# Kernel optimization log

Hardware: AMD Instinct MI355X
Metric: run time of the kernel (lower is better)

The kernel has to match this reference:

```python
import jax, jax.numpy as jnp
import numpy as np

N_NODES = 50000
N_EDGES = 600000
N_GRAPHS = 256
IN_C = 128
HID = 128
OUT_C = 2


def setup_inputs() -> dict:
    key = jax.random.key(0)
    ks = jax.random.split(key, 16)
    d = {}
    d["x"] = jax.random.normal(ks[0], (N_NODES, IN_C), jnp.float32)
    d["edge_index"] = jax.random.randint(ks[1], (2, N_EDGES), 0, N_NODES, dtype=jnp.int32)
    d["root_node_idx"] = jax.random.randint(ks[2], (N_GRAPHS,), 0, N_NODES, dtype=jnp.int32)
    d["batch"] = jnp.sort(jax.random.randint(ks[3], (N_NODES,), 0, N_GRAPHS, dtype=jnp.int32))
    dims = [(IN_C, HID), (HID, HID), (HID, HID), (HID, HID)]
    for i, (ci, co) in enumerate(dims, start=1):
        s = 1.0 / np.sqrt(ci)
        d[f"w{i}_l"] = jax.random.uniform(ks[3 + i], (co, ci), jnp.float32, -s, s)
        d[f"b{i}_l"] = jnp.zeros((co,), jnp.float32)
        d[f"w{i}_r"] = jax.random.uniform(ks[7 + i], (co, ci), jnp.float32, -s, s)
    s = 1.0 / np.sqrt(2 * HID)
    d["w_cls"] = jax.random.uniform(ks[12], (OUT_C, 2 * HID), jnp.float32, -s, s)
    d["b_cls"] = jnp.zeros((OUT_C,), jnp.float32)
    return d


def _sage_conv(x, src, tgt, deg_inv, w_l, b_l, w_r):
    # mean aggregation of source features at target nodes (PyG SAGEConv, aggr='mean')
    agg = jax.ops.segment_sum(x[src], tgt, num_segments=N_NODES) * deg_inv  # [N, C]
    # out = lin_l(agg) + lin_r(x); lin_r has no bias in PyG SAGEConv
    return agg @ w_l.T + b_l + x @ w_r.T


def reference(x, edge_index, root_node_idx, batch,
              w1_l, b1_l, w1_r, w2_l, b2_l, w2_r,
              w3_l, b3_l, w3_r, w4_l, b4_l, w4_r,
              w_cls, b_cls):
    src, tgt = edge_index[0], edge_index[1]
    ones_e = jnp.ones((src.shape[0],), x.dtype)
    deg = jax.ops.segment_sum(ones_e, tgt, num_segments=N_NODES)
    deg_inv = (1.0 / jnp.maximum(deg, 1.0))[:, None]  # [N, 1]

    h = jax.nn.relu(_sage_conv(x, src, tgt, deg_inv, w1_l, b1_l, w1_r))
    h = jax.nn.relu(_sage_conv(h, src, tgt, deg_inv, w2_l, b2_l, w2_r))
    h = jax.nn.relu(_sage_conv(h, src, tgt, deg_inv, w3_l, b3_l, w3_r))
    h = jax.nn.relu(_sage_conv(h, src, tgt, deg_inv, w4_l, b4_l, w4_r))

    root_emb = h[root_node_idx]  # [G, HID]
    g_sum = jax.ops.segment_sum(h, batch, num_segments=N_GRAPHS)
    g_cnt = jax.ops.segment_sum(jnp.ones((h.shape[0],), h.dtype), batch, num_segments=N_GRAPHS)
    graph_emb = g_sum / jnp.maximum(g_cnt, 1.0)[:, None]  # [G, HID]

    combined = jnp.concatenate([root_emb, graph_emb], axis=1)  # [G, 2*HID]
    return combined @ w_cls.T + b_cls  # [G, OUT_C]
```

## Files before the change

kernel.cpp:

```cpp
#include <hip/hip_runtime.h>
#include <hip/hip_bf16.h>

#define N_NODES 50000
#define N_EDGES 600000
#define N_GRAPHS 256
#define C 128
#define NB 196

typedef unsigned short ushort;
typedef unsigned int uint;
typedef __attribute__((ext_vector_type(8))) short bfrag8;
typedef __attribute__((ext_vector_type(4))) float facc4;

__device__ __forceinline__ ushort f2bf(float v) {
    uint u = __float_as_uint(v);
    u += 0x7FFFu + ((u >> 16) & 1u);
    return (ushort)(u >> 16);
}
__device__ __forceinline__ float bf2f(ushort u) {
    return __uint_as_float(((uint)u) << 16);
}
__device__ __forceinline__ void fsplit(float v, ushort& h, ushort& l) {
    h = f2bf(v);
    l = f2bf(v - bf2f(h));
}

__global__ void k_deg(const int* __restrict__ tgt, int* __restrict__ deg) {
    int e = blockIdx.x * blockDim.x + threadIdx.x;
    if (e < N_EDGES) atomicAdd(&deg[tgt[e]], 1);
}

__global__ __launch_bounds__(256) void k_bsum(const int* __restrict__ deg,
                                              int* __restrict__ bsum,
                                              float* __restrict__ dinv) {
    __shared__ int ws[4];
    int idx = blockIdx.x * 256 + threadIdx.x;
    int v = (idx < N_NODES) ? deg[idx] : 0;
    if (idx < N_NODES) dinv[idx] = 1.0f / fmaxf((float)v, 1.0f);
    int s = v;
#pragma unroll
    for (int off = 1; off < 64; off <<= 1) s += __shfl_xor(s, off);
    if ((threadIdx.x & 63) == 0) ws[threadIdx.x >> 6] = s;
    __syncthreads();
    if (threadIdx.x == 0) bsum[blockIdx.x] = ws[0] + ws[1] + ws[2] + ws[3];
}

__global__ __launch_bounds__(256) void k_bscan(const int* __restrict__ bsum,
                                               int* __restrict__ boff,
                                               int* __restrict__ rowptr) {
    __shared__ int ws[4];
    int t = threadIdx.x, lane = t & 63, w = t >> 6;
    int v = (t < NB) ? bsum[t] : 0;
    int incl = v;
#pragma unroll
    for (int off = 1; off < 64; off <<= 1) {
        int u = __shfl_up(incl, off);
        if (lane >= off) incl += u;
    }
    if (lane == 63) ws[w] = incl;
    __syncthreads();
    int wo = 0;
    if (w > 0) wo += ws[0];
    if (w > 1) wo += ws[1];
    if (w > 2) wo += ws[2];
    if (t < NB) boff[t] = wo + incl - v;
    if (t == 0) rowptr[N_NODES] = N_EDGES;
}

__global__ __launch_bounds__(256) void k_rowptr(const int* __restrict__ deg,
                                                const int* __restrict__ boff,
                                                int* __restrict__ rowptr) {
    __shared__ int ws[4];
    int b = blockIdx.x, t = threadIdx.x;
    int idx = b * 256 + t;
    int lane = t & 63, w = t >> 6;
    int v = (idx < N_NODES) ? deg[idx] : 0;
    int incl = v;
#pragma unroll
    for (int off = 1; off < 64; off <<= 1) {
        int u = __shfl_up(incl, off);
        if (lane >= off) incl += u;
    }
    if (lane == 63) ws[w] = incl;
    __syncthreads();
    int wo = 0;
    if (w > 0) wo += ws[0];
    if (w > 1) wo += ws[1];
    if (w > 2) wo += ws[2];
    if (idx < N_NODES) rowptr[idx] = boff[b] + wo + incl - v;
}

__global__ void k_fill(const int* __restrict__ src, const int* __restrict__ tgt,
                       const int* __restrict__ rowptr, int* __restrict__ fill,
                       int* __restrict__ csr_src) {
    int e = blockIdx.x * blockDim.x + threadIdx.x;
    if (e >= N_EDGES) return;
    int d = tgt[e];
    int pos = atomicAdd(&fill[d], 1);
    csr_src[rowptr[d] + pos] = src[e];
}

__global__ __launch_bounds__(256) void k_xsplit(const float* __restrict__ x,
                                                ushort* __restrict__ Ahi,
                                                ushort* __restrict__ Alo) {
    int gid = blockIdx.x * 256 + threadIdx.x;
    if (gid >= N_NODES * 32) return;
    int n = gid >> 5, c4 = (gid & 31) << 2;
    float4 v = *(const float4*)(x + (size_t)n * C + c4);
    ushort4 h, l;
    fsplit(v.x, h.x, l.x); fsplit(v.y, h.y, l.y);
    fsplit(v.z, h.z, l.z); fsplit(v.w, h.w, l.w);
    *(ushort4*)(Ahi + (size_t)n * 256 + 128 + c4) = h;
    *(ushort4*)(Alo + (size_t)n * 256 + 128 + c4) = l;
}

struct WPtrs { const float* wl[4]; const float* wr[4]; };
__global__ __launch_bounds__(256) void k_wsplit(WPtrs wp, ushort* __restrict__ BTh,
                                                ushort* __restrict__ BTl) {
    int gid = blockIdx.x * 256 + threadIdx.x;
    if (gid >= 4 * 128 * 256) return;
    int l = gid >> 15;
    int rem = gid & 32767;
    int n = rem >> 8, k = rem & 255;
    float v = (k < 128) ? wp.wl[l][n * 128 + k] : wp.wr[l][n * 128 + (k - 128)];
    ushort h, lo;
    fsplit(v, h, lo);
    BTh[gid] = h;
    BTl[gid] = lo;
}

__global__ __launch_bounds__(256) void k_gather(const ushort* __restrict__ Ahi_r,
                                                const ushort* __restrict__ Alo_r,
                                                ushort* __restrict__ Ahi_w,
                                                ushort* __restrict__ Alo_w,
                                                const int* __restrict__ csr_src,
                                                const int* __restrict__ rowptr,
                                                const float* __restrict__ dinv) {
    int node = blockIdx.x * 8 + (threadIdx.x >> 5);
    if (node >= N_NODES) return;
    int lane = threadIdx.x & 31;
    int c4 = lane << 2;
    int s = rowptr[node], e = rowptr[node + 1];
    float a0 = 0.f, a1 = 0.f, a2 = 0.f, a3 = 0.f;
    int j = s;
    for (; j + 3 < e; j += 4) {
        int s0 = csr_src[j], s1 = csr_src[j + 1];
        int s2 = csr_src[j + 2], s3 = csr_src[j + 3];
        ushort4 h0 = *(const ushort4*)(Ahi_r + (size_t)s0 * 256 + 128 + c4);
        ushort4 l0 = *(const ushort4*)(Alo_r + (size_t)s0 * 256 + 128 + c4);
        ushort4 h1 = *(const ushort4*)(Ahi_r + (size_t)s1 * 256 + 128 + c4);
        ushort4 l1 = *(const ushort4*)(Alo_r + (size_t)s1 * 256 + 128 + c4);
        ushort4 h2 = *(const ushort4*)(Ahi_r + (size_t)s2 * 256 + 128 + c4);
        ushort4 l2 = *(const ushort4*)(Alo_r + (size_t)s2 * 256 + 128 + c4);
        ushort4 h3 = *(const ushort4*)(Ahi_r + (size_t)s3 * 256 + 128 + c4);
        ushort4 l3 = *(const ushort4*)(Alo_r + (size_t)s3 * 256 + 128 + c4);
        a0 += (bf2f(h0.x) + bf2f(l0.x)) + (bf2f(h1.x) + bf2f(l1.x))
            + (bf2f(h2.x) + bf2f(l2.x)) + (bf2f(h3.x) + bf2f(l3.x));
        a1 += (bf2f(h0.y) + bf2f(l0.y)) + (bf2f(h1.y) + bf2f(l1.y))
            + (bf2f(h2.y) + bf2f(l2.y)) + (bf2f(h3.y) + bf2f(l3.y));
        a2 += (bf2f(h0.z) + bf2f(l0.z)) + (bf2f(h1.z) + bf2f(l1.z))
            + (bf2f(h2.z) + bf2f(l2.z)) + (bf2f(h3.z) + bf2f(l3.z));
        a3 += (bf2f(h0.w) + bf2f(l0.w)) + (bf2f(h1.w) + bf2f(l1.w))
            + (bf2f(h2.w) + bf2f(l2.w)) + (bf2f(h3.w) + bf2f(l3.w));
    }
    for (; j < e; j++) {
        int s0 = csr_src[j];
        ushort4 h0 = *(const ushort4*)(Ahi_r + (size_t)s0 * 256 + 128 + c4);
        ushort4 l0 = *(const ushort4*)(Alo_r + (size_t)s0 * 256 + 128 + c4);
        a0 += bf2f(h0.x) + bf2f(l0.x);
        a1 += bf2f(h0.y) + bf2f(l0.y);
        a2 += bf2f(h0.z) + bf2f(l0.z);
        a3 += bf2f(h0.w) + bf2f(l0.w);
    }
    float sc = dinv[node];
    a0 *= sc; a1 *= sc; a2 *= sc; a3 *= sc;
    ushort4 h, l;
    fsplit(a0, h.x, l.x); fsplit(a1, h.y, l.y);
    fsplit(a2, h.z, l.z); fsplit(a3, h.w, l.w);
    *(ushort4*)(Ahi_w + (size_t)node * 256 + c4) = h;
    *(ushort4*)(Alo_w + (size_t)node * 256 + c4) = l;
}

__global__ __launch_bounds__(256) void k_gemm(const ushort* __restrict__ Ahi,
                                              const ushort* __restrict__ Alo,
                                              const ushort* __restrict__ BTh,
                                              const ushort* __restrict__ BTl,
                                              const float* __restrict__ bl,
                                              ushort* __restrict__ Hhi,
                                              ushort* __restrict__ Hlo) {
    __shared__ short As[2][128][40];
    __shared__ short Bs[2][128][40];
    const int tid = threadIdx.x;
    const int wave = tid >> 6, lane = tid & 63;
    const int m0 = blockIdx.x * 128;
    const int wm = (wave & 1) * 64;
    const int wn = (wave >> 1) * 64;
    const int l15 = lane & 15, lk = (lane >> 4) * 8;

    const int sr = tid >> 1;
    const int sc = (tid & 1) * 16;
    int garow = m0 + sr; if (garow >= N_NODES) garow = N_NODES - 1;
    const ushort* pAh = Ahi + (size_t)garow * 256 + sc;
    const ushort* pAl = Alo + (size_t)garow * 256 + sc;
    const ushort* pBh = BTh + sr * 256 + sc;
    const ushort* pBl = BTl + sr * 256 + sc;

    bfrag8 rAh0, rAh1, rAl0, rAl1, rBh0, rBh1, rBl0, rBl1;
#define LOADSTEP(K0) do { \
        rAh0 = *(const bfrag8*)(pAh + (K0));     rAh1 = *(const bfrag8*)(pAh + (K0) + 8); \
        rAl0 = *(const bfrag8*)(pAl + (K0));     rAl1 = *(const bfrag8*)(pAl + (K0) + 8); \
        rBh0 = *(const bfrag8*)(pBh + (K0));     rBh1 = *(const bfrag8*)(pBh + (K0) + 8); \
        rBl0 = *(const bfrag8*)(pBl + (K0));     rBl1 = *(const bfrag8*)(pBl + (K0) + 8); \
    } while (0)

    LOADSTEP(0);
    facc4 acc[4][4] = {};
#pragma unroll
    for (int s = 0; s < 8; s++) {
        *(bfrag8*)&As[0][sr][sc]     = rAh0;  *(bfrag8*)&As[0][sr][sc + 8] = rAh1;
        *(bfrag8*)&As[1][sr][sc]     = rAl0;  *(bfrag8*)&As[1][sr][sc + 8] = rAl1;
        *(bfrag8*)&Bs[0][sr][sc]     = rBh0;  *(bfrag8*)&Bs[0][sr][sc + 8] = rBh1;
        *(bfrag8*)&Bs[1][sr][sc]     = rBl0;  *(bfrag8*)&Bs[1][sr][sc + 8] = rBl1;
        __syncthreads();
        if (s < 7) LOADSTEP((s + 1) * 32);
        bfrag8 a[2][4], b[2][4];
#pragma unroll
        for (int t = 0; t < 4; t++) {
            a[0][t] = *(const bfrag8*)&As[0][wm + t * 16 + l15][lk];
            a[1][t] = *(const bfrag8*)&As[1][wm + t * 16 + l15][lk];
            b[0][t] = *(const bfrag8*)&Bs[0][wn + t * 16 + l15][lk];
            b[1][t] = *(const bfrag8*)&Bs[1][wn + t * 16 + l15][lk];
        }
#pragma unroll
        for (int mt = 0; mt < 4; mt++)
#pragma unroll
            for (int nt = 0; nt < 4; nt++) {
                acc[mt][nt] = __builtin_amdgcn_mfma_f32_16x16x32_bf16(a[0][mt], b[0][nt], acc[mt][nt], 0, 0, 0);
                acc[mt][nt] = __builtin_amdgcn_mfma_f32_16x16x32_bf16(a[0][mt], b[1][nt], acc[mt][nt], 0, 0, 0);
                acc[mt][nt] = __builtin_amdgcn_mfma_f32_16x16x32_bf16(a[1][mt], b[0][nt], acc[mt][nt], 0, 0, 0);
            }
        __syncthreads();
    }
#undef LOADSTEP

    const int r4 = (lane >> 4) * 4;
#pragma unroll
    for (int mt = 0; mt < 4; mt++) {
#pragma unroll
        for (int nt = 0; nt < 4; nt++) {
            int col = wn + nt * 16 + l15;
            float bias = bl[col];
#pragma unroll
            for (int r = 0; r < 4; r++) {
                int grow = m0 + wm + mt * 16 + r4 + r;
                if (grow < N_NODES) {
                    float v = fmaxf(acc[mt][nt][r] + bias, 0.f);
                    ushort h, l;
                    fsplit(v, h, l);
                    Hhi[(size_t)grow * 256 + 128 + col] = h;
                    Hlo[(size_t)grow * 256 + 128 + col] = l;
                }
            }
        }
    }
}

__global__ void k_gstart(const int* __restrict__ batch, int* __restrict__ gstart) {
    int g = blockIdx.x * blockDim.x + threadIdx.x;
    if (g > N_GRAPHS) return;
    int lo = 0, hi = N_NODES;
    while (lo < hi) {
        int mid = (lo + hi) >> 1;
        if (batch[mid] < g) lo = mid + 1;
        else hi = mid;
    }
    gstart[g] = lo;
}

__global__ __launch_bounds__(512) void k_pool(const ushort* __restrict__ Ahi,
                                              const ushort* __restrict__ Alo,
                                              const int* __restrict__ gstart,
                                              float* __restrict__ gmean) {
    __shared__ float part[4][C];
    int g = blockIdx.x;
    int c = threadIdx.x & 127, p = threadIdx.x >> 7;
    int s = gstart[g], e = gstart[g + 1];
    float sum = 0.f;
    for (int n = s + p; n < e; n += 4) {
        size_t o = (size_t)n * 256 + 128 + c;
        sum += bf2f(Ahi[o]) + bf2f(Alo[o]);
    }
    part[p][c] = sum;
    __syncthreads();
    if (p == 0) {
        float tot = part[0][c] + part[1][c] + part[2][c] + part[3][c];
        float cnt = fmaxf((float)(e - s), 1.0f);
        gmean[g * C + c] = tot / cnt;
    }
}

__global__ __launch_bounds__(256) void k_final(const ushort* __restrict__ Ahi,
                                               const ushort* __restrict__ Alo,
                                               const float* __restrict__ gmean,
                                               const int* __restrict__ root,
                                               const float* __restrict__ wcls,
                                               const float* __restrict__ bcls,
                                               float* __restrict__ out) {
    __shared__ float red[8];
    int g = blockIdx.x, t = threadIdx.x;
    float v;
    if (t < 128) {
        size_t o = (size_t)root[g] * 256 + 128 + t;
        v = bf2f(Ahi[o]) + bf2f(Alo[o]);
    } else {
        v = gmean[g * C + (t - 128)];
    }
    float p0 = v * wcls[t];
    float p1 = v * wcls[256 + t];
#pragma unroll
    for (int off = 32; off; off >>= 1) {
        p0 += __shfl_down(p0, off);
        p1 += __shfl_down(p1, off);
    }
    int wid = t >> 6;
    if ((t & 63) == 0) { red[wid] = p0; red[4 + wid] = p1; }
    __syncthreads();
    if (t == 0) {
        out[g * 2 + 0] = red[0] + red[1] + red[2] + red[3] + bcls[0];
        out[g * 2 + 1] = red[4] + red[5] + red[6] + red[7] + bcls[1];
    }
}

extern "C" void kernel_launch(void* const* d_in, const int* in_sizes, int n_in,
                              void* d_out, int out_size, void* d_ws, size_t ws_size,
                              hipStream_t stream) {
    const float* x = (const float*)d_in[0];
    const int* ei = (const int*)d_in[1];
    const int* src = ei;
    const int* tgt = ei + N_EDGES;
    const int* root = (const int*)d_in[2];
    const int* batch = (const int*)d_in[3];
    WPtrs wp;
    wp.wl[0] = (const float*)d_in[4];  wp.wr[0] = (const float*)d_in[6];
    wp.wl[1] = (const float*)d_in[7];  wp.wr[1] = (const float*)d_in[9];
    wp.wl[2] = (const float*)d_in[10]; wp.wr[2] = (const float*)d_in[12];
    wp.wl[3] = (const float*)d_in[13]; wp.wr[3] = (const float*)d_in[15];
    const float* blv[4] = {(const float*)d_in[5], (const float*)d_in[8],
                           (const float*)d_in[11], (const float*)d_in[14]};
    const float* wcls = (const float*)d_in[16];
    const float* bcls = (const float*)d_in[17];
    float* out = (float*)d_out;

    ushort* Ahi = (ushort*)d_ws;
    ushort* Alo = Ahi + (size_t)N_NODES * 256;
    ushort* BTh = Alo + (size_t)N_NODES * 256;
    ushort* BTl = BTh + 4 * 128 * 256;
    int* deg = (int*)(BTl + 4 * 128 * 256);
    float* dinv = (float*)(deg + N_NODES);
    int* rowptr = (int*)(dinv + N_NODES);
    int* fill = rowptr + N_NODES + 1;
    int* csr_src = fill + N_NODES;
    int* bsum = csr_src + N_EDGES;
    int* boff = bsum + 256;
    int* gstart = boff + 256;
    float* gmean = (float*)(gstart + 260);

    hipMemsetAsync(deg, 0, N_NODES * sizeof(int), stream);
    hipMemsetAsync(fill, 0, N_NODES * sizeof(int), stream);
    k_deg<<<(N_EDGES + 255) / 256, 256, 0, stream>>>(tgt, deg);
    k_bsum<<<NB, 256, 0, stream>>>(deg, bsum, dinv);
    k_bscan<<<1, 256, 0, stream>>>(bsum, boff, rowptr);
    k_rowptr<<<NB, 256, 0, stream>>>(deg, boff, rowptr);
    k_fill<<<(N_EDGES + 255) / 256, 256, 0, stream>>>(src, tgt, rowptr, fill, csr_src);
    k_gstart<<<1, 512, 0, stream>>>(batch, gstart);
    k_xsplit<<<(N_NODES * 32 + 255) / 256, 256, 0, stream>>>(x, Ahi, Alo);
    k_wsplit<<<(4 * 128 * 256 + 255) / 256, 256, 0, stream>>>(wp, BTh, BTl);

    for (int l = 0; l < 4; l++) {
        k_gather<<<(N_NODES + 7) / 8, 256, 0, stream>>>(Ahi, Alo, Ahi, Alo,
                                                        csr_src, rowptr, dinv);
        k_gemm<<<(N_NODES + 127) / 128, 256, 0, stream>>>(
            Ahi, Alo, BTh + l * 32768, BTl + l * 32768, blv[l], Ahi, Alo);
    }
    k_pool<<<N_GRAPHS, 512, 0, stream>>>(Ahi, Alo, gstart, gmean);
    k_final<<<N_GRAPHS, 256, 0, stream>>>(Ahi, Alo, gmean, root, wcls, bcls, out);
}
```

Measured before the change: 486.4 us.

## Widen gather loads to 16 bytes and restage GEMM A tiles in MFMA fragment order

```diff
diff --git a/kernel.cpp b/kernel.cpp
--- a/kernel.cpp
+++ b/kernel.cpp
@@ -136,49 +136,50 @@
                                                 const int* __restrict__ csr_src,
                                                 const int* __restrict__ rowptr,
                                                 const float* __restrict__ dinv) {
-    int node = blockIdx.x * 8 + (threadIdx.x >> 5);
+    int node = blockIdx.x * 16 + (threadIdx.x >> 4);
     if (node >= N_NODES) return;
-    int lane = threadIdx.x & 31;
-    int c4 = lane << 2;
+    int c8 = (threadIdx.x & 15) << 3;
     int s = rowptr[node], e = rowptr[node + 1];
-    float a0 = 0.f, a1 = 0.f, a2 = 0.f, a3 = 0.f;
+    float a[8] = {0.f, 0.f, 0.f, 0.f, 0.f, 0.f, 0.f, 0.f};
     int j = s;
     for (; j + 3 < e; j += 4) {
         int s0 = csr_src[j], s1 = csr_src[j + 1];
         int s2 = csr_src[j + 2], s3 = csr_src[j + 3];
-        ushort4 h0 = *(const ushort4*)(Ahi_r + (size_t)s0 * 256 + 128 + c4);
-        ushort4 l0 = *(const ushort4*)(Alo_r + (size_t)s0 * 256 + 128 + c4);
-        ushort4 h1 = *(const ushort4*)(Ahi_r + (size_t)s1 * 256 + 128 + c4);
-        ushort4 l1 = *(const ushort4*)(Alo_r + (size_t)s1 * 256 + 128 + c4);
-        ushort4 h2 = *(const ushort4*)(Ahi_r + (size_t)s2 * 256 + 128 + c4);
-        ushort4 l2 = *(const ushort4*)(Alo_r + (size_t)s2 * 256 + 128 + c4);
-        ushort4 h3 = *(const ushort4*)(Ahi_r + (size_t)s3 * 256 + 128 + c4);
-        ushort4 l3 = *(const ushort4*)(Alo_r + (size_t)s3 * 256 + 128 + c4);
-        a0 += (bf2f(h0.x) + bf2f(l0.x)) + (bf2f(h1.x) + bf2f(l1.x))
-            + (bf2f(h2.x) + bf2f(l2.x)) + (bf2f(h3.x) + bf2f(l3.x));
-        a1 += (bf2f(h0.y) + bf2f(l0.y)) + (bf2f(h1.y) + bf2f(l1.y))
-            + (bf2f(h2.y) + bf2f(l2.y)) + (bf2f(h3.y) + bf2f(l3.y));
-        a2 += (bf2f(h0.z) + bf2f(l0.z)) + (bf2f(h1.z) + bf2f(l1.z))
-            + (bf2f(h2.z) + bf2f(l2.z)) + (bf2f(h3.z) + bf2f(l3.z));
-        a3 += (bf2f(h0.w) + bf2f(l0.w)) + (bf2f(h1.w) + bf2f(l1.w))
-            + (bf2f(h2.w) + bf2f(l2.w)) + (bf2f(h3.w) + bf2f(l3.w));
+        bfrag8 h0 = *(const bfrag8*)(Ahi_r + (size_t)s0 * 256 + 128 + c8);
+        bfrag8 l0 = *(const bfrag8*)(Alo_r + (size_t)s0 * 256 + 128 + c8);
+        bfrag8 h1 = *(const bfrag8*)(Ahi_r + (size_t)s1 * 256 + 128 + c8);
+        bfrag8 l1 = *(const bfrag8*)(Alo_r + (size_t)s1 * 256 + 128 + c8);
+        bfrag8 h2 = *(const bfrag8*)(Ahi_r + (size_t)s2 * 256 + 128 + c8);
+        bfrag8 l2 = *(const bfrag8*)(Alo_r + (size_t)s2 * 256 + 128 + c8);
+        bfrag8 h3 = *(const bfrag8*)(Ahi_r + (size_t)s3 * 256 + 128 + c8);
+        bfrag8 l3 = *(const bfrag8*)(Alo_r + (size_t)s3 * 256 + 128 + c8);
+#pragma unroll
+        for (int c = 0; c < 8; c++)
+            a[c] += (bf2f((ushort)h0[c]) + bf2f((ushort)l0[c]))
+                  + (bf2f((ushort)h1[c]) + bf2f((ushort)l1[c]))
+                  + (bf2f((ushort)h2[c]) + bf2f((ushort)l2[c]))
+                  + (bf2f((ushort)h3[c]) + bf2f((ushort)l3[c]));
     }
     for (; j < e; j++) {
         int s0 = csr_src[j];
-        ushort4 h0 = *(const ushort4*)(Ahi_r + (size_t)s0 * 256 + 128 + c4);
-        ushort4 l0 = *(const ushort4*)(Alo_r + (size_t)s0 * 256 + 128 + c4);
-        a0 += bf2f(h0.x) + bf2f(l0.x);
-        a1 += bf2f(h0.y) + bf2f(l0.y);
-        a2 += bf2f(h0.z) + bf2f(l0.z);
-        a3 += bf2f(h0.w) + bf2f(l0.w);
+        bfrag8 h0 = *(const bfrag8*)(Ahi_r + (size_t)s0 * 256 + 128 + c8);
+        bfrag8 l0 = *(const bfrag8*)(Alo_r + (size_t)s0 * 256 + 128 + c8);
+#pragma unroll
+        for (int c = 0; c < 8; c++)
+            a[c] += bf2f((ushort)h0[c]) + bf2f((ushort)l0[c]);
     }
     float sc = dinv[node];
-    a0 *= sc; a1 *= sc; a2 *= sc; a3 *= sc;
-    ushort4 h, l;
-    fsplit(a0, h.x, l.x); fsplit(a1, h.y, l.y);
-    fsplit(a2, h.z, l.z); fsplit(a3, h.w, l.w);
-    *(ushort4*)(Ahi_w + (size_t)node * 256 + c4) = h;
-    *(ushort4*)(Alo_w + (size_t)node * 256 + c4) = l;
+    bfrag8 oh, ol;
+#pragma unroll
+    for (int c = 0; c < 8; c++) {
+        float v = a[c] * sc;
+        ushort hh, ll;
+        fsplit(v, hh, ll);
+        oh[c] = (short)hh;
+        ol[c] = (short)ll;
+    }
+    *(bfrag8*)(Ahi_w + (size_t)node * 256 + c8) = oh;
+    *(bfrag8*)(Alo_w + (size_t)node * 256 + c8) = ol;
 }
 
 __global__ __launch_bounds__(256) void k_gemm(const ushort* __restrict__ Ahi,
@@ -188,8 +189,7 @@
                                               const float* __restrict__ bl,
                                               ushort* __restrict__ Hhi,
                                               ushort* __restrict__ Hlo) {
-    __shared__ short As[2][128][40];
-    __shared__ short Bs[2][128][40];
+    __shared__ __align__(16) short As[2][4096];
     const int tid = threadIdx.x;
     const int wave = tid >> 6, lane = tid & 63;
     const int m0 = blockIdx.x * 128;
@@ -197,39 +197,57 @@
     const int wn = (wave >> 1) * 64;
     const int l15 = lane & 15, lk = (lane >> 4) * 8;
 
-    const int sr = tid >> 1;
-    const int sc = (tid & 1) * 16;
-    int garow = m0 + sr; if (garow >= N_NODES) garow = N_NODES - 1;
-    const ushort* pAh = Ahi + (size_t)garow * 256 + sc;
-    const ushort* pAl = Alo + (size_t)garow * 256 + sc;
-    const ushort* pBh = BTh + sr * 256 + sc;
-    const ushort* pBl = BTl + sr * 256 + sc;
-
-    bfrag8 rAh0, rAh1, rAl0, rAl1, rBh0, rBh1, rBl0, rBl1;
+    const ushort* sp[4];
+    short* dp[4];
+#pragma unroll
+    for (int i = 0; i < 4; i++) {
+        int gid = tid + i * 256;
+        int p = gid >> 9, rem = gid & 511;
+        int mt = rem >> 6, c = rem & 63;
+        int row = m0 + mt * 16 + (c & 15);
+        if (row >= N_NODES) row = N_NODES - 1;
+        sp[i] = (p ? Alo : Ahi) + (size_t)row * 256 + ((c >> 4) << 3);
+        dp[i] = &As[p][mt * 512 + c * 8];
+    }
+    const ushort* pBh[4];
+    const ushort* pBl[4];
+#pragma unroll
+    for (int t = 0; t < 4; t++) {
+        int n = wn + t * 16 + l15;
+        pBh[t] = BTh + n * 256 + lk;
+        pBl[t] = BTl + n * 256 + lk;
+    }
+
+    bfrag8 r[4];
 #define LOADSTEP(K0) do { \
-        rAh0 = *(const bfrag8*)(pAh + (K0));     rAh1 = *(const bfrag8*)(pAh + (K0) + 8); \
-        rAl0 = *(const bfrag8*)(pAl + (K0));     rAl1 = *(const bfrag8*)(pAl + (K0) + 8); \
-        rBh0 = *(const bfrag8*)(pBh + (K0));     rBh1 = *(const bfrag8*)(pBh + (K0) + 8); \
-        rBl0 = *(const bfrag8*)(pBl + (K0));     rBl1 = *(const bfrag8*)(pBl + (K0) + 8); \
+        r[0] = *(const bfrag8*)(sp[0] + (K0)); \
+        r[1] = *(const bfrag8*)(sp[1] + (K0)); \
+        r[2] = *(const bfrag8*)(sp[2] + (K0)); \
+        r[3] = *(const bfrag8*)(sp[3] + (K0)); \
     } while (0)
 
     LOADSTEP(0);
     facc4 acc[4][4] = {};
 #pragma unroll
     for (int s = 0; s < 8; s++) {
-        *(bfrag8*)&As[0][sr][sc]     = rAh0;  *(bfrag8*)&As[0][sr][sc + 8] = rAh1;
-        *(bfrag8*)&As[1][sr][sc]     = rAl0;  *(bfrag8*)&As[1][sr][sc + 8] = rAl1;
-        *(bfrag8*)&Bs[0][sr][sc]     = rBh0;  *(bfrag8*)&Bs[0][sr][sc + 8] = rBh1;
-        *(bfrag8*)&Bs[1][sr][sc]     = rBl0;  *(bfrag8*)&Bs[1][sr][sc + 8] = rBl1;
+        *(bfrag8*)dp[0] = r[0];
+        *(bfrag8*)dp[1] = r[1];
+        *(bfrag8*)dp[2] = r[2];
+        *(bfrag8*)dp[3] = r[3];
         __syncthreads();
         if (s < 7) LOADSTEP((s + 1) * 32);
-        bfrag8 a[2][4], b[2][4];
+        const int k0 = s * 32;
+        bfrag8 b[2][4], a[2][4];
 #pragma unroll
         for (int t = 0; t < 4; t++) {
-            a[0][t] = *(const bfrag8*)&As[0][wm + t * 16 + l15][lk];
-            a[1][t] = *(const bfrag8*)&As[1][wm + t * 16 + l15][lk];
-            b[0][t] = *(const bfrag8*)&Bs[0][wn + t * 16 + l15][lk];
-            b[1][t] = *(const bfrag8*)&Bs[1][wn + t * 16 + l15][lk];
+            b[0][t] = *(const bfrag8*)(pBh[t] + k0);
+            b[1][t] = *(const bfrag8*)(pBl[t] + k0);
+        }
+#pragma unroll
+        for (int t = 0; t < 4; t++) {
+            int mt = (wm >> 4) + t;
+            a[0][t] = *(const bfrag8*)&As[0][mt * 512 + lane * 8];
+            a[1][t] = *(const bfrag8*)&As[1][mt * 512 + lane * 8];
         }
 #pragma unroll
         for (int mt = 0; mt < 4; mt++)
@@ -251,10 +269,10 @@
             int col = wn + nt * 16 + l15;
             float bias = bl[col];
 #pragma unroll
-            for (int r = 0; r < 4; r++) {
-                int grow = m0 + wm + mt * 16 + r4 + r;
+            for (int rr = 0; rr < 4; rr++) {
+                int grow = m0 + wm + mt * 16 + r4 + rr;
                 if (grow < N_NODES) {
-                    float v = fmaxf(acc[mt][nt][r] + bias, 0.f);
+                    float v = fmaxf(acc[mt][nt][rr] + bias, 0.f);
                     ushort h, l;
                     fsplit(v, h, l);
                     Hhi[(size_t)grow * 256 + 128 + col] = h;
@@ -377,8 +395,8 @@
     k_wsplit<<<(4 * 128 * 256 + 255) / 256, 256, 0, stream>>>(wp, BTh, BTl);
 
     for (int l = 0; l < 4; l++) {
-        k_gather<<<(N_NODES + 7) / 8, 256, 0, stream>>>(Ahi, Alo, Ahi, Alo,
-                                                        csr_src, rowptr, dinv);
+        k_gather<<<(N_NODES + 15) / 16, 256, 0, stream>>>(Ahi, Alo, Ahi, Alo,
+                                                          csr_src, rowptr, dinv);
         k_gemm<<<(N_NODES + 127) / 128, 256, 0, stream>>>(
             Ahi, Alo, BTh + l * 32768, BTl + l * 32768, blv[l], Ahi, Alo);
     }
```

Result: slower. 523.7 us (+7.7%).
